# Kernel optimization log

Measured on AMD Instinct MI355X. Metric: run time of the kernel, lower is better.

## Reference

```python
import jax, jax.numpy as jnp
import numpy as np

GAMMA = 0.95        # gamma_lemma: persistence decay per cycle (eq. 12.1)
KAPPA = 0.1         # kappa_interfere: lateral interference strength (eq. 12.3)
T_STEPS = 50        # t_lemma_steps: integration window before selection (eq. 12.2)
FLOOR = 1e-6        # confidence_floor for peak-to-average ratio

B, N_CONCEPTS, N_LEMMAS = 4096, 1024, 512


def setup_inputs() -> dict:
    key = jax.random.key(0)
    k1, k2 = jax.random.split(key, 2)
    # kernel boundary hands in a normalized concept distribution
    c_raw = jax.random.uniform(k1, (B, N_CONCEPTS), dtype=jnp.float32)
    c_lex = c_raw / jnp.sum(c_raw, axis=-1, keepdims=True)
    # TiedSubstrate W_C_to_L: (out_dim=n_lemmas, in_dim=n_concepts)
    W = jax.random.normal(k2, (N_LEMMAS, N_CONCEPTS), dtype=jnp.float32) / np.sqrt(N_CONCEPTS)
    # persistent lemma activation buffer a_lemma, zero at reset
    a0 = jnp.zeros((B, N_LEMMAS), dtype=jnp.float32)
    return {"c_lex": c_lex, "W": W, "a0": a0}


def reference(c_lex, W, a0):
    """Integrate lemma activations for T_STEPS cycles, then select.

    Per cycle (eq. 12.1 + 12.3):
      a <- gamma * a + c_lex @ W^T            # decay + concept->lemma drive
      a <- a - kappa * (sum_j a_j - a)        # lateral interference from other lemmas
      a <- max(a, 0)                          # rectify activations
    Selection (eq. 12.2): argmax over lemmas; confidence = peak / max(mean, floor).
    """
    def step(a, _):
        a = GAMMA * a + jnp.einsum('bc,lc->bl', c_lex, W)   # (B, n_lemmas)
        a = a - KAPPA * (jnp.sum(a, axis=-1, keepdims=True) - a)
        a = jnp.maximum(a, 0.0)
        return a, None

    a, _ = jax.lax.scan(step, a0, None, length=T_STEPS)
    peak = jnp.max(a, axis=-1)
    mean = jnp.mean(a, axis=-1)
    confidence = peak / jnp.maximum(mean, FLOOR)
    selected = jnp.argmax(a, axis=-1)
    return a, selected, confidence
```

## Files before the change

kernel.cpp:

```cpp
#include <hip/hip_runtime.h>
#include <hip/hip_bf16.h>

#define BATCH 4096
#define NC    1024
#define NL    512
#define TSTEPS 50
#define GAMMA_C 0.95f
#define KAPPA_C 0.1f
#define FLOOR_C 1e-6f

typedef __attribute__((ext_vector_type(8))) short short8;
typedef __attribute__((ext_vector_type(4))) float f32x4;

__device__ __forceinline__ void split2_pk(float x0, float x1,
                                          unsigned& hp, unsigned& lp) {
    union { __hip_bfloat162 b; unsigned u; } ch, cl;
    ch.b = __float22bfloat162_rn(make_float2(x0, x1));
    hp = ch.u;
    const float hf0 = __uint_as_float(hp << 16);
    const float hf1 = __uint_as_float(hp & 0xFFFF0000u);
    cl.b = __float22bfloat162_rn(make_float2(x0 - hf0, x1 - hf1));
    lp = cl.u;
}

#define W_FLOATS (NL * NC)
#define W_BLOCKS (W_FLOATS / (256 * 8))
#define A_BLOCKS ((BATCH * NC) / (256 * 8))

__global__ __launch_bounds__(256)
void convert_hilo(const float* __restrict__ W, const float* __restrict__ A,
                  unsigned short* __restrict__ Whi, unsigned short* __restrict__ Wlo,
                  unsigned short* __restrict__ Ahi, unsigned short* __restrict__ Alo) {
    const int b = blockIdx.x;
    const float* src;
    unsigned short *dh, *dl;
    if (b < W_BLOCKS) {
        const size_t fidx = ((size_t)b * 256 + threadIdx.x) * 8;
        src = W + fidx; dh = Whi + fidx; dl = Wlo + fidx;
    } else {
        const size_t fidx = ((size_t)(b - W_BLOCKS) * 256 + threadIdx.x) * 8;
        src = A + fidx; dh = Ahi + fidx; dl = Alo + fidx;
    }
    const float4 v0 = ((const float4*)src)[0];
    const float4 v1 = ((const float4*)src)[1];
    uint4 h, l;
    split2_pk(v0.x, v0.y, h.x, l.x);
    split2_pk(v0.z, v0.w, h.y, l.y);
    split2_pk(v1.x, v1.y, h.z, l.z);
    split2_pk(v1.z, v1.w, h.w, l.w);
    *(uint4*)dh = h;
    *(uint4*)dl = l;
}

__device__ __forceinline__ float wave_sum_bcast(float x) {
    float f = x;
    f += __int_as_float(__builtin_amdgcn_update_dpp(
            0, __float_as_int(f), 0x111, 0xf, 0xf, true));
    f += __int_as_float(__builtin_amdgcn_update_dpp(
            0, __float_as_int(f), 0x112, 0xf, 0xf, true));
    f += __int_as_float(__builtin_amdgcn_update_dpp(
            0, __float_as_int(f), 0x114, 0xf, 0xf, true));
    f += __int_as_float(__builtin_amdgcn_update_dpp(
            0, __float_as_int(f), 0x118, 0xf, 0xf, true));
    f += __int_as_float(__builtin_amdgcn_update_dpp(
            0, __float_as_int(f), 0x142, 0xa, 0xf, true));
    f += __int_as_float(__builtin_amdgcn_update_dpp(
            0, __float_as_int(f), 0x143, 0xc, 0xf, true));
    return __int_as_float(__builtin_amdgcn_readlane(__float_as_int(f), 63));
}

__device__ __forceinline__ void glds16(const unsigned short* g, unsigned short* l) {
    __builtin_amdgcn_global_load_lds(
        (__attribute__((address_space(1))) void*)(g),
        (__attribute__((address_space(3))) void*)(l), 16, 0, 0);
}

#define TM 128
#define TN 128
#define GK 32
#define SPLITK 2
#define NST (NC / SPLITK / GK)

__global__ __launch_bounds__(256)
void gemm_bf16x2(const unsigned short* __restrict__ Ahi, const unsigned short* __restrict__ Alo,
                 const unsigned short* __restrict__ Whi, const unsigned short* __restrict__ Wlo,
                 float* __restrict__ Dp) {
    __shared__ unsigned short S[2][4][TM * GK];

    const int tid  = threadIdx.x;
    const int lane = tid & 63;
    const int w    = tid >> 6;
    const int m0 = blockIdx.x * TM;
    const int n0 = blockIdx.y * TN;
    const int kb = blockIdx.z * (NC / SPLITK);

    const int srow = w * 32 + (lane >> 2);
    const int scol = (lane & 3) * 8;
    const unsigned short* gAh = Ahi + (size_t)(m0 + srow) * NC + kb + scol;
    const unsigned short* gAl = Alo + (size_t)(m0 + srow) * NC + kb + scol;
    const unsigned short* gBh = Whi + (size_t)(n0 + srow) * NC + kb + scol;
    const unsigned short* gBl = Wlo + (size_t)(n0 + srow) * NC + kb + scol;
    const int ld0 = (w * 32) * GK + lane * 8;

    const int mw   = (w >> 1) * 64;
    const int nw   = (w & 1) * 64;
    const int sr   = lane & 15;
    const int quad = lane >> 4;
    const int rA = (mw + sr) * GK + quad * 8;
    const int rB = (nw + sr) * GK + quad * 8;

    f32x4 acc[4][4];
    #pragma unroll
    for (int i = 0; i < 4; ++i)
        #pragma unroll
        for (int j = 0; j < 4; ++j)
            acc[i][j] = (f32x4){0.f, 0.f, 0.f, 0.f};

    #define STAGE(buf, kofs)                                          \
        {                                                             \
            const int ko = (kofs);                                    \
            glds16(gAh + ko,           &S[buf][0][ld0]);              \
            glds16(gAh + ko + 16 * NC, &S[buf][0][ld0 + 16 * GK]);    \
            glds16(gAl + ko,           &S[buf][1][ld0]);              \
            glds16(gAl + ko + 16 * NC, &S[buf][1][ld0 + 16 * GK]);    \
            glds16(gBh + ko,           &S[buf][2][ld0]);              \
            glds16(gBh + ko + 16 * NC, &S[buf][2][ld0 + 16 * GK]);    \
            glds16(gBl + ko,           &S[buf][3][ld0]);              \
            glds16(gBl + ko + 16 * NC, &S[buf][3][ld0 + 16 * GK]);    \
        }

    #define KSTEP(CUR, VM, DO_STAGE, NEXTK)                                    \
        {                                                                      \
            asm volatile("s_waitcnt vmcnt(" #VM ")" ::: "memory");             \
            __builtin_amdgcn_sched_barrier(0);                                 \
            __builtin_amdgcn_s_barrier();                                      \
            __builtin_amdgcn_sched_barrier(0);                                 \
            short8 afh[4], afl[4], bfh[4], bfl[4];                             \
            _Pragma("unroll")                                                  \
            for (int mi = 0; mi < 4; ++mi) {                                   \
                afh[mi] = *(const short8*)&S[CUR][0][rA + mi * 16 * GK];       \
                afl[mi] = *(const short8*)&S[CUR][1][rA + mi * 16 * GK];       \
            }                                                                  \
            _Pragma("unroll")                                                  \
            for (int ni = 0; ni < 4; ++ni) {                                   \
                bfh[ni] = *(const short8*)&S[CUR][2][rB + ni * 16 * GK];       \
                bfl[ni] = *(const short8*)&S[CUR][3][rB + ni * 16 * GK];       \
            }                                                                  \
            _Pragma("unroll")                                                  \
            for (int mi = 0; mi < 4; ++mi) {                                   \
                _Pragma("unroll")                                              \
                for (int ni = 0; ni < 4; ++ni) {                               \
                    acc[mi][ni] = __builtin_amdgcn_mfma_f32_16x16x32_bf16(     \
                        afh[mi], bfh[ni], acc[mi][ni], 0, 0, 0);               \
                    acc[mi][ni] = __builtin_amdgcn_mfma_f32_16x16x32_bf16(     \
                        afh[mi], bfl[ni], acc[mi][ni], 0, 0, 0);               \
                    acc[mi][ni] = __builtin_amdgcn_mfma_f32_16x16x32_bf16(     \
                        afl[mi], bfh[ni], acc[mi][ni], 0, 0, 0);               \
                }                                                              \
            }                                                                  \
            __builtin_amdgcn_sched_barrier(0);                                 \
            __builtin_amdgcn_s_barrier();                                      \
            __builtin_amdgcn_sched_barrier(0);                                 \
            if (DO_STAGE) STAGE(CUR, NEXTK);                                   \
        }

    STAGE(0, 0);
    STAGE(1, GK);

    #pragma unroll 2
    for (int s = 0; s < NST - 2; ++s)
        KSTEP((s & 1), 8, true, (s + 2) * GK);
    KSTEP(0, 8, false, 0);
    KSTEP(1, 0, false, 0);

    float* Dz = Dp + (size_t)blockIdx.z * BATCH * NL;
    #pragma unroll
    for (int mi = 0; mi < 4; ++mi) {
        #pragma unroll
        for (int ni = 0; ni < 4; ++ni) {
            const int col = n0 + nw + ni * 16 + sr;
            #pragma unroll
            for (int r = 0; r < 4; ++r) {
                const int row = m0 + mw + mi * 16 + quad * 4 + r;
                Dz[(size_t)row * NL + col] = acc[mi][ni][r];
            }
        }
    }
}

template<int SK>
__global__ __launch_bounds__(256)
void iterate_select(const float* __restrict__ Dp,
                    float* __restrict__ a_out,
                    float* __restrict__ sel_out, float* __restrict__ conf_out) {
    const int lane = threadIdx.x & 63;
    const int wave = threadIdx.x >> 6;
    const int row  = blockIdx.x * 4 + wave;

    float d[8];
    {
        float4 v[SK][2];
        #pragma unroll
        for (int s = 0; s < SK; ++s) {
            const float4* ps = (const float4*)(Dp + (size_t)s * BATCH * NL
                                               + (size_t)row * NL + lane * 8);
            v[s][0] = ps[0];
            v[s][1] = ps[1];
        }
        d[0] = v[0][0].x; d[1] = v[0][0].y; d[2] = v[0][0].z; d[3] = v[0][0].w;
        d[4] = v[0][1].x; d[5] = v[0][1].y; d[6] = v[0][1].z; d[7] = v[0][1].w;
        #pragma unroll
        for (int s = 1; s < SK; ++s) {
            d[0] += v[s][0].x; d[1] += v[s][0].y; d[2] += v[s][0].z; d[3] += v[s][0].w;
            d[4] += v[s][1].x; d[5] += v[s][1].y; d[6] += v[s][1].z; d[7] += v[s][1].w;
        }
    }

    float a[8];
    #pragma unroll
    for (int j = 0; j < 8; ++j) a[j] = 0.f;

    const float K1 = 1.0f + KAPPA_C;

    for (int t = 0; t < TSTEPS; ++t) {
        #pragma unroll
        for (int j = 0; j < 8; ++j) a[j] = fmaf(GAMMA_C, a[j], d[j]);

        float t4a = a[0] + a[4], t4b = a[1] + a[5], t4c = a[2] + a[6], t4d = a[3] + a[7];
        float t2a = t4a + t4c, t2b = t4b + t4d;
        const float S = wave_sum_bcast(t2a + t2b);

        const float h = -KAPPA_C * S;
        #pragma unroll
        for (int j = 0; j < 8; ++j) {
            const float v = fmaf(K1, a[j], h);
            a[j] = v > 0.f ? v : 0.f;
        }
    }

    float m4a = fmaxf(a[0], a[4]), m4b = fmaxf(a[1], a[5]);
    float m4c = fmaxf(a[2], a[6]), m4d = fmaxf(a[3], a[7]);
    float peak = fmaxf(fmaxf(m4a, m4b), fmaxf(m4c, m4d));
    float s4a = a[0] + a[4], s4b = a[1] + a[5], s4c = a[2] + a[6], s4d = a[3] + a[7];
    float ssum = wave_sum_bcast((s4a + s4b) + (s4c + s4d));

    #pragma unroll
    for (int m = 1; m < 64; m <<= 1)
        peak = fmaxf(peak, __shfl_xor(peak, m, 64));

    const float mean = ssum * (1.0f / (float)NL);
    const float conf = peak / fmaxf(mean, FLOOR_C);

    int idx = 0x7fffffff;
    #pragma unroll
    for (int j = 0; j < 8; ++j)
        if (a[j] == peak) idx = min(idx, lane * 8 + j);
    #pragma unroll
    for (int m = 1; m < 64; m <<= 1)
        idx = min(idx, __shfl_xor(idx, m, 64));

    float4* ar = (float4*)(a_out + (size_t)row * NL + lane * 8);
    float4 o0, o1;
    o0.x = a[0]; o0.y = a[1]; o0.z = a[2]; o0.w = a[3];
    o1.x = a[4]; o1.y = a[5]; o1.z = a[6]; o1.w = a[7];
    ar[0] = o0; ar[1] = o1;

    if (lane == 0) {
        if (sel_out)  sel_out[row]  = (float)idx;
        if (conf_out) conf_out[row] = conf;
    }
}

extern "C" void kernel_launch(void* const* d_in, const int* in_sizes, int n_in,
                              void* d_out, int out_size, void* d_ws, size_t ws_size,
                              hipStream_t stream) {
    const float* c_lex = (const float*)d_in[0];
    const float* W     = (const float*)d_in[1];

    float* D = (float*)d_ws;
    unsigned short* Whi = (unsigned short*)(D + (size_t)SPLITK * BATCH * NL);
    unsigned short* Wlo = Whi + (size_t)NL * NC;
    unsigned short* Ahi = Wlo + (size_t)NL * NC;
    unsigned short* Alo = Ahi + (size_t)BATCH * NC;

    float* a_out = (float*)d_out;
    float* sel   = nullptr;
    float* conf  = nullptr;
    const int base = BATCH * NL;
    if (out_size >= base + 2 * BATCH) {
        sel  = a_out + base;
        conf = a_out + base + BATCH;
    } else if (out_size >= base + BATCH) {
        conf = a_out + base;
    }

    convert_hilo<<<dim3(W_BLOCKS + A_BLOCKS), 256, 0, stream>>>(
        W, c_lex, Whi, Wlo, Ahi, Alo);

    gemm_bf16x2<<<dim3(BATCH / TM, NL / TN, SPLITK), 256, 0, stream>>>(
        Ahi, Alo, Whi, Wlo, D);

    iterate_select<SPLITK><<<dim3(BATCH / 4), 256, 0, stream>>>(D, a_out, sel, conf);
}
```

Measured before the change: 109.8 us.

## Fuse convert, GEMM, and iteration into one cooperative persistent kernel

Replaces the three launches (hi/lo bf16 split, split-K GEMM, iterate/select) with a single cooperative kernel of 256 blocks that uses grid-wide syncs between phases. The GEMM tile changes to 128x64 with no split-K, so each block covers the full K loop and the partial-sum reduction goes away. Each wave then integrates four rows instead of one. This is meant to remove launch gaps and the split-K traffic, at the cost of only 256 blocks on the GPU, two grid barriers, and a longer serial K loop per block. The old three-kernel path remains as a fallback if the cooperative launch fails.

```diff
diff --git a/kernel.cpp b/kernel.cpp
--- a/kernel.cpp
+++ b/kernel.cpp
@@ -1,5 +1,8 @@
 #include <hip/hip_runtime.h>
 #include <hip/hip_bf16.h>
+#include <hip/hip_cooperative_groups.h>
+
+namespace cg = cooperative_groups;
 
 #define BATCH 4096
 #define NC    1024
@@ -21,35 +24,6 @@
     const float hf1 = __uint_as_float(hp & 0xFFFF0000u);
     cl.b = __float22bfloat162_rn(make_float2(x0 - hf0, x1 - hf1));
     lp = cl.u;
-}
-
-#define W_FLOATS (NL * NC)
-#define W_BLOCKS (W_FLOATS / (256 * 8))
-#define A_BLOCKS ((BATCH * NC) / (256 * 8))
-
-__global__ __launch_bounds__(256)
-void convert_hilo(const float* __restrict__ W, const float* __restrict__ A,
-                  unsigned short* __restrict__ Whi, unsigned short* __restrict__ Wlo,
-                  unsigned short* __restrict__ Ahi, unsigned short* __restrict__ Alo) {
-    const int b = blockIdx.x;
-    const float* src;
-    unsigned short *dh, *dl;
-    if (b < W_BLOCKS) {
-        const size_t fidx = ((size_t)b * 256 + threadIdx.x) * 8;
-        src = W + fidx; dh = Whi + fidx; dl = Wlo + fidx;
-    } else {
-        const size_t fidx = ((size_t)(b - W_BLOCKS) * 256 + threadIdx.x) * 8;
-        src = A + fidx; dh = Ahi + fidx; dl = Alo + fidx;
-    }
-    const float4 v0 = ((const float4*)src)[0];
-    const float4 v1 = ((const float4*)src)[1];
-    uint4 h, l;
-    split2_pk(v0.x, v0.y, h.x, l.x);
-    split2_pk(v0.z, v0.w, h.y, l.y);
-    split2_pk(v1.x, v1.y, h.z, l.z);
-    split2_pk(v1.z, v1.w, h.w, l.w);
-    *(uint4*)dh = h;
-    *(uint4*)dl = l;
 }
 
 __device__ __forceinline__ float wave_sum_bcast(float x) {
@@ -76,22 +50,276 @@
 }
 
 #define TM 128
-#define TN 128
+#define TN 64
 #define GK 32
+#define FNST (NC / GK)
+
+__global__ __launch_bounds__(256)
+void fused_all(const float* __restrict__ A, const float* __restrict__ W,
+               unsigned short* __restrict__ Whi, unsigned short* __restrict__ Wlo,
+               unsigned short* __restrict__ Ahi, unsigned short* __restrict__ Alo,
+               float* __restrict__ D,
+               float* __restrict__ a_out, float* __restrict__ sel_out,
+               float* __restrict__ conf_out) {
+    __shared__ unsigned short S[2][12288];
+
+    const int tid  = threadIdx.x;
+    const int lane = tid & 63;
+    const int w    = tid >> 6;
+    const int l    = blockIdx.x;
+    const int mi_b = (l & 7) + 8 * (l >> 6);
+    const int ni_b = (l >> 3) & 7;
+
+    {
+        const size_t wofs = (size_t)l * 2048 + tid * 8;
+        const float4 w0 = *(const float4*)(W + wofs);
+        const float4 w1 = *(const float4*)(W + wofs + 4);
+        uint4 h, lo;
+        split2_pk(w0.x, w0.y, h.x, lo.x);
+        split2_pk(w0.z, w0.w, h.y, lo.y);
+        split2_pk(w1.x, w1.y, h.z, lo.z);
+        split2_pk(w1.z, w1.w, h.w, lo.w);
+        *(uint4*)(Whi + wofs) = h;
+        *(uint4*)(Wlo + wofs) = lo;
+
+        const int r0A = mi_b * 128 + ni_b * 16;
+        #pragma unroll
+        for (int c = 0; c < 8; ++c) {
+            const int row = r0A + c * 2 + (tid >> 7);
+            const int col = (tid & 127) * 8;
+            const size_t idx = (size_t)row * NC + col;
+            const float4 a0 = *(const float4*)(A + idx);
+            const float4 a1 = *(const float4*)(A + idx + 4);
+            uint4 hh, ll;
+            split2_pk(a0.x, a0.y, hh.x, ll.x);
+            split2_pk(a0.z, a0.w, hh.y, ll.y);
+            split2_pk(a1.x, a1.y, hh.z, ll.z);
+            split2_pk(a1.z, a1.w, hh.w, ll.w);
+            *(uint4*)(Ahi + idx) = hh;
+            *(uint4*)(Alo + idx) = ll;
+        }
+    }
+    __threadfence();
+    cg::this_grid().sync();
+
+    const int m0 = mi_b * TM;
+    const int n0 = ni_b * TN;
+
+    const unsigned short* gAh = Ahi + (size_t)(m0 + w * 32 + (lane >> 2)) * NC + (lane & 3) * 8;
+    const unsigned short* gAl = Alo + (size_t)(m0 + w * 32 + (lane >> 2)) * NC + (lane & 3) * 8;
+    const unsigned short* gBh = Whi + (size_t)(n0 + w * 16 + (lane >> 2)) * NC + (lane & 3) * 8;
+    const unsigned short* gBl = Wlo + (size_t)(n0 + w * 16 + (lane >> 2)) * NC + (lane & 3) * 8;
+    const int ald = w * 1024 + lane * 8;
+    const int bld = w * 512  + lane * 8;
+
+    const int sr   = lane & 15;
+    const int quad = lane >> 4;
+    const int mw = (w >> 1) * 64;
+    const int nw = (w & 1) * 32;
+    const int rA = (mw + sr) * GK + quad * 8;
+    const int rB = (nw + sr) * GK + quad * 8;
+
+    f32x4 acc[4][2];
+    #pragma unroll
+    for (int i = 0; i < 4; ++i)
+        #pragma unroll
+        for (int j = 0; j < 2; ++j)
+            acc[i][j] = (f32x4){0.f, 0.f, 0.f, 0.f};
+
+    #define FSTAGE(buf, kofs)                                         \
+        {                                                             \
+            const int ko = (kofs);                                    \
+            glds16(gAh + ko,           &S[buf][ald]);                 \
+            glds16(gAh + ko + 16 * NC, &S[buf][ald + 512]);           \
+            glds16(gAl + ko,           &S[buf][4096 + ald]);          \
+            glds16(gAl + ko + 16 * NC, &S[buf][4096 + ald + 512]);    \
+            glds16(gBh + ko,           &S[buf][8192 + bld]);          \
+            glds16(gBl + ko,           &S[buf][10240 + bld]);         \
+        }
+
+    #define FKSTEP(CUR, VMSTR, DO_STAGE, NEXTK)                                \
+        {                                                                      \
+            asm volatile("s_waitcnt vmcnt(" VMSTR ")" ::: "memory");           \
+            __builtin_amdgcn_sched_barrier(0);                                 \
+            __builtin_amdgcn_s_barrier();                                      \
+            __builtin_amdgcn_sched_barrier(0);                                 \
+            short8 afh[4], afl[4], bfh[2], bfl[2];                             \
+            _Pragma("unroll")                                                  \
+            for (int mi = 0; mi < 4; ++mi) {                                   \
+                afh[mi] = *(const short8*)&S[CUR][rA + mi * 512];              \
+                afl[mi] = *(const short8*)&S[CUR][4096 + rA + mi * 512];       \
+            }                                                                  \
+            _Pragma("unroll")                                                  \
+            for (int ni = 0; ni < 2; ++ni) {                                   \
+                bfh[ni] = *(const short8*)&S[CUR][8192 + rB + ni * 512];       \
+                bfl[ni] = *(const short8*)&S[CUR][10240 + rB + ni * 512];      \
+            }                                                                  \
+            _Pragma("unroll")                                                  \
+            for (int mi = 0; mi < 4; ++mi) {                                   \
+                _Pragma("unroll")                                              \
+                for (int ni = 0; ni < 2; ++ni) {                               \
+                    acc[mi][ni] = __builtin_amdgcn_mfma_f32_16x16x32_bf16(     \
+                        afh[mi], bfh[ni], acc[mi][ni], 0, 0, 0);               \
+                    acc[mi][ni] = __builtin_amdgcn_mfma_f32_16x16x32_bf16(     \
+                        afh[mi], bfl[ni], acc[mi][ni], 0, 0, 0);               \
+                    acc[mi][ni] = __builtin_amdgcn_mfma_f32_16x16x32_bf16(     \
+                        afl[mi], bfh[ni], acc[mi][ni], 0, 0, 0);               \
+                }                                                              \
+            }                                                                  \
+            __builtin_amdgcn_sched_barrier(0);                                 \
+            __builtin_amdgcn_s_barrier();                                      \
+            __builtin_amdgcn_sched_barrier(0);                                 \
+            if (DO_STAGE) FSTAGE(CUR, NEXTK);                                  \
+        }
+
+    FSTAGE(0, 0);
+    FSTAGE(1, GK);
+    #pragma unroll 2
+    for (int s = 0; s < FNST - 2; ++s)
+        FKSTEP((s & 1), "6", true, (s + 2) * GK);
+    FKSTEP(0, "6", false, 0);
+    FKSTEP(1, "0", false, 0);
+
+    #pragma unroll
+    for (int mi2 = 0; mi2 < 4; ++mi2) {
+        #pragma unroll
+        for (int ni2 = 0; ni2 < 2; ++ni2) {
+            const int col = n0 + nw + ni2 * 16 + sr;
+            #pragma unroll
+            for (int r = 0; r < 4; ++r) {
+                const int row = m0 + mw + mi2 * 16 + quad * 4 + r;
+                D[(size_t)row * NL + col] = acc[mi2][ni2][r];
+            }
+        }
+    }
+    __threadfence();
+    cg::this_grid().sync();
+
+    const int r0 = l * 16 + w * 4;
+    float d[4][8];
+    #pragma unroll
+    for (int rr = 0; rr < 4; ++rr) {
+        const float4 u0 = *(const float4*)(D + (size_t)(r0 + rr) * NL + lane * 8);
+        const float4 u1 = *(const float4*)(D + (size_t)(r0 + rr) * NL + lane * 8 + 4);
+        d[rr][0] = u0.x; d[rr][1] = u0.y; d[rr][2] = u0.z; d[rr][3] = u0.w;
+        d[rr][4] = u1.x; d[rr][5] = u1.y; d[rr][6] = u1.z; d[rr][7] = u1.w;
+    }
+
+    float a[4][8];
+    #pragma unroll
+    for (int rr = 0; rr < 4; ++rr)
+        #pragma unroll
+        for (int j = 0; j < 8; ++j) a[rr][j] = 0.f;
+
+    const float K1 = 1.0f + KAPPA_C;
+    for (int t = 0; t < TSTEPS; ++t) {
+        #pragma unroll
+        for (int rr = 0; rr < 4; ++rr)
+            #pragma unroll
+            for (int j = 0; j < 8; ++j)
+                a[rr][j] = fmaf(GAMMA_C, a[rr][j], d[rr][j]);
+
+        float Sv[4];
+        #pragma unroll
+        for (int rr = 0; rr < 4; ++rr) {
+            float t4a = a[rr][0] + a[rr][4], t4b = a[rr][1] + a[rr][5];
+            float t4c = a[rr][2] + a[rr][6], t4d = a[rr][3] + a[rr][7];
+            Sv[rr] = wave_sum_bcast((t4a + t4c) + (t4b + t4d));
+        }
+        #pragma unroll
+        for (int rr = 0; rr < 4; ++rr) {
+            const float h = -KAPPA_C * Sv[rr];
+            #pragma unroll
+            for (int j = 0; j < 8; ++j) {
+                const float v = fmaf(K1, a[rr][j], h);
+                a[rr][j] = v > 0.f ? v : 0.f;
+            }
+        }
+    }
+
+    #pragma unroll
+    for (int rr = 0; rr < 4; ++rr) {
+        const int row = r0 + rr;
+        float m4a = fmaxf(a[rr][0], a[rr][4]), m4b = fmaxf(a[rr][1], a[rr][5]);
+        float m4c = fmaxf(a[rr][2], a[rr][6]), m4d = fmaxf(a[rr][3], a[rr][7]);
+        float peak = fmaxf(fmaxf(m4a, m4b), fmaxf(m4c, m4d));
+        float s4a = a[rr][0] + a[rr][4], s4b = a[rr][1] + a[rr][5];
+        float s4c = a[rr][2] + a[rr][6], s4d = a[rr][3] + a[rr][7];
+        float ssum = wave_sum_bcast((s4a + s4b) + (s4c + s4d));
+
+        #pragma unroll
+        for (int m = 1; m < 64; m <<= 1)
+            peak = fmaxf(peak, __shfl_xor(peak, m, 64));
+
+        const float mean = ssum * (1.0f / (float)NL);
+        const float conf = peak / fmaxf(mean, FLOOR_C);
+
+        int idx = 0x7fffffff;
+        #pragma unroll
+        for (int j = 0; j < 8; ++j)
+            if (a[rr][j] == peak) idx = min(idx, lane * 8 + j);
+        #pragma unroll
+        for (int m = 1; m < 64; m <<= 1)
+            idx = min(idx, __shfl_xor(idx, m, 64));
+
+        float4 o0, o1;
+        o0.x = a[rr][0]; o0.y = a[rr][1]; o0.z = a[rr][2]; o0.w = a[rr][3];
+        o1.x = a[rr][4]; o1.y = a[rr][5]; o1.z = a[rr][6]; o1.w = a[rr][7];
+        float4* arp = (float4*)(a_out + (size_t)row * NL + lane * 8);
+        arp[0] = o0; arp[1] = o1;
+
+        if (lane == 0) {
+            if (sel_out)  sel_out[row]  = (float)idx;
+            if (conf_out) conf_out[row] = conf;
+        }
+    }
+}
+
+#define W_FLOATS (NL * NC)
+#define W_BLOCKS (W_FLOATS / (256 * 8))
+#define A_BLOCKS ((BATCH * NC) / (256 * 8))
+
+__global__ __launch_bounds__(256)
+void convert_hilo(const float* __restrict__ W, const float* __restrict__ A,
+                  unsigned short* __restrict__ Whi, unsigned short* __restrict__ Wlo,
+                  unsigned short* __restrict__ Ahi, unsigned short* __restrict__ Alo) {
+    const int b = blockIdx.x;
+    const float* src;
+    unsigned short *dh, *dl;
+    if (b < W_BLOCKS) {
+        const size_t fidx = ((size_t)b * 256 + threadIdx.x) * 8;
+        src = W + fidx; dh = Whi + fidx; dl = Wlo + fidx;
+    } else {
+        const size_t fidx = ((size_t)(b - W_BLOCKS) * 256 + threadIdx.x) * 8;
+        src = A + fidx; dh = Ahi + fidx; dl = Alo + fidx;
+    }
+    const float4 v0 = ((const float4*)src)[0];
+    const float4 v1 = ((const float4*)src)[1];
+    uint4 h, l;
+    split2_pk(v0.x, v0.y, h.x, l.x);
+    split2_pk(v0.z, v0.w, h.y, l.y);
+    split2_pk(v1.x, v1.y, h.z, l.z);
+    split2_pk(v1.z, v1.w, h.w, l.w);
+    *(uint4*)dh = h;
+    *(uint4*)dl = l;
+}
+
+#define TM3 128
+#define TN3 128
 #define SPLITK 2
-#define NST (NC / SPLITK / GK)
+#define NST3 (NC / SPLITK / GK)
 
 __global__ __launch_bounds__(256)
 void gemm_bf16x2(const unsigned short* __restrict__ Ahi, const unsigned short* __restrict__ Alo,
                  const unsigned short* __restrict__ Whi, const unsigned short* __restrict__ Wlo,
                  float* __restrict__ Dp) {
-    __shared__ unsigned short S[2][4][TM * GK];
+    __shared__ unsigned short S[2][4][TM3 * GK];
 
     const int tid  = threadIdx.x;
     const int lane = tid & 63;
     const int w    = tid >> 6;
-    const int m0 = blockIdx.x * TM;
-    const int n0 = blockIdx.y * TN;
+    const int m0 = blockIdx.x * TM3;
+    const int n0 = blockIdx.y * TN3;
     const int kb = blockIdx.z * (NC / SPLITK);
 
     const int srow = w * 32 + (lane >> 2);
@@ -116,7 +344,7 @@
         for (int j = 0; j < 4; ++j)
             acc[i][j] = (f32x4){0.f, 0.f, 0.f, 0.f};
 
-    #define STAGE(buf, kofs)                                          \
+    #define STAGE3(buf, kofs)                                         \
         {                                                             \
             const int ko = (kofs);                                    \
             glds16(gAh + ko,           &S[buf][0][ld0]);              \
@@ -129,9 +357,9 @@
             glds16(gBl + ko + 16 * NC, &S[buf][3][ld0 + 16 * GK]);    \
         }
 
-    #define KSTEP(CUR, VM, DO_STAGE, NEXTK)                                    \
+    #define KSTEP3(CUR, VMSTR, DO_STAGE, NEXTK)                                \
         {                                                                      \
-            asm volatile("s_waitcnt vmcnt(" #VM ")" ::: "memory");             \
+            asm volatile("s_waitcnt vmcnt(" VMSTR ")" ::: "memory");           \
             __builtin_amdgcn_sched_barrier(0);                                 \
             __builtin_amdgcn_s_barrier();                                      \
             __builtin_amdgcn_sched_barrier(0);                                 \
@@ -161,17 +389,16 @@
             __builtin_amdgcn_sched_barrier(0);                                 \
             __builtin_amdgcn_s_barrier();                                      \
             __builtin_amdgcn_sched_barrier(0);                                 \
-            if (DO_STAGE) STAGE(CUR, NEXTK);                                   \
-        }
-
-    STAGE(0, 0);
-    STAGE(1, GK);
-
+            if (DO_STAGE) STAGE3(CUR, NEXTK);                                  \
+        }
+
+    STAGE3(0, 0);
+    STAGE3(1, GK);
     #pragma unroll 2
-    for (int s = 0; s < NST - 2; ++s)
-        KSTEP((s & 1), 8, true, (s + 2) * GK);
-    KSTEP(0, 8, false, 0);
-    KSTEP(1, 0, false, 0);
+    for (int s = 0; s < NST3 - 2; ++s)
+        KSTEP3((s & 1), "8", true, (s + 2) * GK);
+    KSTEP3(0, "8", false, 0);
+    KSTEP3(1, "0", false, 0);
 
     float* Dz = Dp + (size_t)blockIdx.z * BATCH * NL;
     #pragma unroll
@@ -219,17 +446,13 @@
     float a[8];
     #pragma unroll
     for (int j = 0; j < 8; ++j) a[j] = 0.f;
-
     const float K1 = 1.0f + KAPPA_C;
 
     for (int t = 0; t < TSTEPS; ++t) {
         #pragma unroll
         for (int j = 0; j < 8; ++j) a[j] = fmaf(GAMMA_C, a[j], d[j]);
-
         float t4a = a[0] + a[4], t4b = a[1] + a[5], t4c = a[2] + a[6], t4d = a[3] + a[7];
-        float t2a = t4a + t4c, t2b = t4b + t4d;
-        const float S = wave_sum_bcast(t2a + t2b);
-
+        const float S = wave_sum_bcast((t4a + t4c) + (t4b + t4d));
         const float h = -KAPPA_C * S;
         #pragma unroll
         for (int j = 0; j < 8; ++j) {
@@ -278,7 +501,7 @@
     const float* W     = (const float*)d_in[1];
 
     float* D = (float*)d_ws;
-    unsigned short* Whi = (unsigned short*)(D + (size_t)SPLITK * BATCH * NL);
+    unsigned short* Whi = (unsigned short*)(D + 2ull * BATCH * NL);
     unsigned short* Wlo = Whi + (size_t)NL * NC;
     unsigned short* Ahi = Wlo + (size_t)NL * NC;
     unsigned short* Alo = Ahi + (size_t)BATCH * NC;
@@ -294,11 +517,18 @@
         conf = a_out + base;
     }
 
-    convert_hilo<<<dim3(W_BLOCKS + A_BLOCKS), 256, 0, stream>>>(
-        W, c_lex, Whi, Wlo, Ahi, Alo);
-
-    gemm_bf16x2<<<dim3(BATCH / TM, NL / TN, SPLITK), 256, 0, stream>>>(
-        Ahi, Alo, Whi, Wlo, D);
-
-    iterate_select<SPLITK><<<dim3(BATCH / 4), 256, 0, stream>>>(D, a_out, sel, conf);
-}
+    void* args[] = {(void*)&c_lex, (void*)&W, (void*)&Whi, (void*)&Wlo,
+                    (void*)&Ahi, (void*)&Alo, (void*)&D,
+                    (void*)&a_out, (void*)&sel, (void*)&conf};
+    hipError_t e = hipLaunchCooperativeKernel((const void*)fused_all,
+                                              dim3(256), dim3(256),
+                                              args, 0, stream);
+    if (e != hipSuccess) {
+        convert_hilo<<<dim3(W_BLOCKS + A_BLOCKS), 256, 0, stream>>>(
+            W, c_lex, Whi, Wlo, Ahi, Alo);
+        gemm_bf16x2<<<dim3(BATCH / TM3, NL / TN3, SPLITK), 256, 0, stream>>>(
+            Ahi, Alo, Whi, Wlo, D);
+        iterate_select<SPLITK><<<dim3(BATCH / 4), 256, 0, stream>>>(
+            D, a_out, sel, conf);
+    }
+}
```

New measurement: 232.3 us. 111% more time.
